# Kernel optimization log

Measured on AMD Instinct MI355X. Metric: run time of the kernel, lower is better.

## Reference

```python
import jax, jax.numpy as jnp
import numpy as np

B, C_IN, C_OUT, K, H, W = 8, 512, 512, 3, 32, 32
EPS = 1e-8


def _fir_filter():
    f1 = jnp.array([1.0, 3.0, 3.0, 1.0], dtype=jnp.float32)
    f = jnp.outer(f1, f1)
    f = f / f.sum()
    return f * 4.0  # gain = 2**2, filter.ndim/2 == 1


def setup_inputs() -> dict:
    key = jax.random.key(0)
    k1, k2, k3 = jax.random.split(key, 3)
    x = jax.random.normal(k1, (B, C_IN, H, W), dtype=jnp.float32)
    styles = jax.random.normal(k2, (B, C_IN), dtype=jnp.float32)
    w = jax.random.normal(k3, (C_OUT, C_IN, K, K), dtype=jnp.float32)  # lr_multiplier=1
    return {"x": x, "styles": styles, "w": w}


def reference(x, styles, w):
    batch = x.shape[0]
    gain = 1.0 / np.sqrt(C_OUT * C_IN * K * K)
    # modulate: [B, O, I, kh, kw]
    wm = (w[None] * gain) * (styles[:, None, :, None, None] + 1.0)
    # demodulate
    dcoefs = jax.lax.rsqrt(jnp.sum(wm * wm, axis=(2, 3, 4)) + EPS)  # [B, O]
    wm = wm * dcoefs[:, :, None, None, None]
    # fused modconv: batch folded into channels/groups
    x1 = x.reshape(1, batch * C_IN, H, W)
    # torch conv_transpose2d(stride=2, padding=0, groups=B) == dilated conv with
    # spatially flipped kernel, lhs_dilation=2, padding=K-1 on each side.
    w_eq = jnp.flip(wm, axis=(-2, -1)).reshape(batch * C_OUT, C_IN, K, K)
    y = jax.lax.conv_general_dilated(
        x1, w_eq,
        window_strides=(1, 1),
        padding=[(K - 1, K - 1), (K - 1, K - 1)],
        lhs_dilation=(2, 2),
        feature_group_count=batch,
        dimension_numbers=("NCHW", "OIHW", "NCHW"),
    )  # [1, B*O, 2H+1, 2W+1]
    # Upfirdn2d: up=1, down=1, pad=[1,1,1,1], depthwise 4x4 FIR (cross-correlation;
    # filter is symmetric so no flip needed)
    C = batch * C_OUT
    f = jnp.broadcast_to(_fir_filter()[None, None], (C, 1, 4, 4))
    y = jax.lax.conv_general_dilated(
        y, f,
        window_strides=(1, 1),
        padding=[(1, 1), (1, 1)],
        feature_group_count=C,
        dimension_numbers=("NCHW", "OIHW", "NCHW"),
    )  # [1, B*O, 2H, 2W]
    return y.reshape(batch, C_OUT, 2 * H, 2 * W)
```

## Files before the change

### kernel.cpp

```cpp
#include <hip/hip_runtime.h>
#include <stdint.h>


#define DI __device__ __forceinline__

typedef __bf16 bf16x8 __attribute__((ext_vector_type(8)));
typedef float f32x4 __attribute__((ext_vector_type(4)));

DI float bf2f(ushort u) { union { uint32_t i; float f; } v; v.i = ((uint32_t)u) << 16; return v.f; }
DI ushort f2bf(float f) {
  union { float f; uint32_t i; } v; v.f = f;
  uint32_t x = v.i;
  return (ushort)((x + 0x7FFFu + ((x >> 16) & 1u)) >> 16);
}

#define GAIN (1.0f / 1536.0f)

__global__ __launch_bounds__(256) void k_wprep(const float* __restrict__ w,
                                               const float* __restrict__ styles,
                                               ushort* __restrict__ Wm) {
  const int o = blockIdx.x;
  const int t = threadIdx.x;
  __shared__ float ss[4096];
  __shared__ float dc[8];
  __shared__ float wred[4][8];
#pragma unroll
  for (int j = 0; j < 4; j++) {
    const int idx = (t + j * 256) * 4;
    *(float4*)&ss[idx] = *(const float4*)&styles[idx];
  }
  float wreg[18];
  const float* wp = w + o * 4608 + t * 18;
#pragma unroll
  for (int k = 0; k < 9; k++) {
    float2 v2 = *(const float2*)(wp + 2 * k);
    wreg[2 * k] = v2.x;
    wreg[2 * k + 1] = v2.y;
  }
  float q0 = 0.f, q1 = 0.f;
#pragma unroll
  for (int k = 0; k < 9; k++) {
    q0 += wreg[k] * wreg[k];
    q1 += wreg[9 + k] * wreg[9 + k];
  }
  __syncthreads();
  float pb[8];
#pragma unroll
  for (int b = 0; b < 8; b++) {
    float s0 = ss[b * 512 + 2 * t] + 1.0f;
    float s1 = ss[b * 512 + 2 * t + 1] + 1.0f;
    pb[b] = s0 * s0 * q0 + s1 * s1 * q1;
  }
#pragma unroll
  for (int b = 0; b < 8; b++)
#pragma unroll
    for (int off = 32; off > 0; off >>= 1) pb[b] += __shfl_down(pb[b], off, 64);
  const int wid = t >> 6, lane = t & 63;
  if (lane == 0) {
#pragma unroll
    for (int b = 0; b < 8; b++) wred[wid][b] = pb[b];
  }
  __syncthreads();
  if (t < 8)
    dc[t] = rsqrtf((wred[0][t] + wred[1][t] + wred[2][t] + wred[3][t]) * (GAIN * GAIN) + 1e-8f);
  __syncthreads();
#pragma unroll
  for (int b = 0; b < 8; b++) {
    const float d = dc[b];
    const float s0 = GAIN * (ss[b * 512 + 2 * t] + 1.0f) * d;
    const float s1 = GAIN * (ss[b * 512 + 2 * t + 1] + 1.0f) * d;
    ushort* base = Wm + ((size_t)(b * 9) * 512 + o) * 512 + 2 * t;
#pragma unroll
    for (int tap = 0; tap < 9; tap++) {
      ushort2 val = make_ushort2(f2bf(wreg[tap] * s0), f2bf(wreg[9 + tap] * s1));
      *(ushort2*)(base + (size_t)tap * 262144) = val;
    }
  }
}

__global__ __launch_bounds__(256) void k_xt(const float* __restrict__ x,
                                            ushort* __restrict__ xt) {
  __shared__ float tl[32][257];
  const int b = blockIdx.z, i0 = blockIdx.y * 32, hw0 = blockIdx.x * 256;
  const int t = threadIdx.x;
  const float* xb = x + b * (512 * 1024);
#pragma unroll
  for (int p = 0; p < 8; p++) {
    const int r = p * 4 + (t >> 6);
    const int c4 = (t & 63) * 4;
    float4 v = *(const float4*)&xb[(i0 + r) * 1024 + hw0 + c4];
    tl[r][c4] = v.x; tl[r][c4 + 1] = v.y; tl[r][c4 + 2] = v.z; tl[r][c4 + 3] = v.w;
  }
  __syncthreads();
  ushort* xtb = xt + b * (1024 * 512);
#pragma unroll
  for (int p = 0; p < 8; p++) {
    const int hw = p * 32 + (t >> 3);
    const int i4 = (t & 7) * 4;
    ushort4 v = make_ushort4(f2bf(tl[i4][hw]), f2bf(tl[i4 + 1][hw]),
                             f2bf(tl[i4 + 2][hw]), f2bf(tl[i4 + 3][hw]));
    *(ushort4*)&xtb[(hw0 + hw) * 512 + i0 + i4] = v;
  }
}

__global__ __launch_bounds__(256) void k_gemm(const ushort* __restrict__ A,
                                              const ushort* __restrict__ Bt,
                                              ushort* __restrict__ C) {
  __shared__ __attribute__((aligned(16))) char smem[32768];
  const int id = blockIdx.x;
  const int batch = id & 7;
  const int rem = id >> 3;
  const int tap = rem >> 5;
  const int t = rem & 31;
  const int mt = t >> 3, nt = t & 7;
  const int g = batch * 9 + tap;
  const ushort* Ag = A + g * (512 * 512);
  const ushort* Bg = Bt + batch * (1024 * 512);
  ushort* Cg = C + g * (512 * 1024);
  const int tid = threadIdx.x;
  const int lane = tid & 63, wv = tid >> 6;
  const int m0 = mt * 128, n0 = nt * 128;
  const int wm2 = wv >> 1, wn2 = wv & 1;
  const int lq = lane >> 4, l15 = lane & 15;
  const int l4 = lane & 3, ld4 = lane >> 2;
  const int r0 = (0 * 4 + wv) * 16 + ld4;
  const int r1 = (1 * 4 + wv) * 16 + ld4;

  const ushort* pA0 = Ag + (m0 + r0) * 512 + l4 * 8;
  const ushort* pA1 = Ag + (m0 + r1) * 512 + l4 * 8;
  const ushort* pB0 = Bg + (n0 + r0) * 512 + l4 * 8;
  const ushort* pB1 = Bg + (n0 + r1) * 512 + l4 * 8;
  char* dA0 = smem + (0 * 4 + wv) * 1024;
  char* dA1 = smem + (1 * 4 + wv) * 1024;
  char* dB0 = smem + 8192 + (0 * 4 + wv) * 1024;
  char* dB1 = smem + 8192 + (1 * 4 + wv) * 1024;

#define ISSUE(buf, kc)                                                                        \
  do {                                                                                        \
    __builtin_amdgcn_global_load_lds((const __attribute__((address_space(1))) void*)(pA0 + (kc)), \
                                     (__attribute__((address_space(3))) void*)(dA0 + (buf)*16384), 16, 0, 0); \
    __builtin_amdgcn_global_load_lds((const __attribute__((address_space(1))) void*)(pA1 + (kc)), \
                                     (__attribute__((address_space(3))) void*)(dA1 + (buf)*16384), 16, 0, 0); \
    __builtin_amdgcn_global_load_lds((const __attribute__((address_space(1))) void*)(pB0 + (kc)), \
                                     (__attribute__((address_space(3))) void*)(dB0 + (buf)*16384), 16, 0, 0); \
    __builtin_amdgcn_global_load_lds((const __attribute__((address_space(1))) void*)(pB1 + (kc)), \
                                     (__attribute__((address_space(3))) void*)(dB1 + (buf)*16384), 16, 0, 0); \
  } while (0)

  const char* abase = smem + (wm2 * 64 + l15) * 64 + lq * 16;
  const char* bbase = smem + 8192 + (wn2 * 64 + l15) * 64 + lq * 16;

  f32x4 zero = {0.f, 0.f, 0.f, 0.f};
  f32x4 acc[4][4];
#pragma unroll
  for (int mi = 0; mi < 4; mi++)
#pragma unroll
    for (int ni = 0; ni < 4; ni++) acc[mi][ni] = zero;

  ISSUE(0, 0);
  for (int it = 0; it < 16; ++it) {
    __syncthreads();
    const int cur = it & 1;
    if (it < 15) ISSUE(cur ^ 1, (it + 1) * 32);
    const int bo = cur * 16384;
    bf16x8 af[4], bfr[4];
#pragma unroll
    for (int mi = 0; mi < 4; mi++) af[mi] = *(const bf16x8*)(abase + bo + mi * 1024);
#pragma unroll
    for (int ni = 0; ni < 4; ni++) bfr[ni] = *(const bf16x8*)(bbase + bo + ni * 1024);
#pragma unroll
    for (int mi = 0; mi < 4; mi++)
#pragma unroll
      for (int ni = 0; ni < 4; ni++)
        acc[mi][ni] = __builtin_amdgcn_mfma_f32_16x16x32_bf16(af[mi], bfr[ni], acc[mi][ni], 0, 0, 0);
  }
#undef ISSUE
  __syncthreads();
  ushort* cs = (ushort*)smem;
#pragma unroll
  for (int mi = 0; mi < 4; mi++) {
#pragma unroll
    for (int ni = 0; ni < 4; ni++) {
      const int row = wm2 * 64 + mi * 16 + lq * 4;
      const int col = wn2 * 64 + ni * 16 + l15;
      f32x4 v = acc[mi][ni];
#pragma unroll
      for (int r = 0; r < 4; r++) cs[(row + r) * 128 + col] = f2bf(v[r]);
    }
  }
  __syncthreads();
#pragma unroll
  for (int p = 0; p < 8; p++) {
    const int r2 = p * 16 + (tid >> 4);
    const int c8 = (tid & 15) * 8;
    *(uint4*)(Cg + (m0 + r2) * 1024 + n0 + c8) = *(const uint4*)(cs + r2 * 128 + c8);
  }
}

__global__ __launch_bounds__(256) void k_fir(const ushort* __restrict__ C,
                                             float* __restrict__ out) {
  const int bo = blockIdx.x;
  const int b = bo >> 9, o = bo & 511;
  __shared__ __attribute__((aligned(16))) ushort Ct[9 * 1024];
  __shared__ float V[3 * 64 * 32];
  const ushort* Cb = C + ((size_t)(b * 9) * 512 + o) * 1024;
  for (int c = threadIdx.x; c < 1152; c += 256) {
    const int tap = c >> 7, off = (c & 127) * 8;
    *(uint4*)&Ct[tap * 1024 + off] = *(const uint4*)&Cb[(size_t)tap * 524288 + off];
  }
  __syncthreads();
#pragma unroll
  for (int j = 0; j < 6; j++) {
    const int gidx = threadIdx.x + j * 256;
    const int kw = gidx >> 9;
    const int rem = gidx & 511;
    const int u = rem >> 3;
    const int w0 = (rem & 7) * 4;
    float a0 = 0.f, a1 = 0.f, a2 = 0.f, a3 = 0.f;
#pragma unroll
    for (int kh = 0; kh < 3; kh++) {
      const int s0 = (kh + 1 + u) & 1;
#pragma unroll
      for (int d = 0; d < 2; d++) {
        const int h = (u + s0 + 2 * d - 1 - kh) >> 1;
        const bool ok = (h >= 0) & (h < 32);
        const float cf = ok ? ((s0 == d) ? 1.f : 3.f) : 0.f;
        const int hh = ok ? h : 0;
        const uint2 cv = *(const uint2*)&Ct[kh * 3072 + kw * 1024 + hh * 32 + w0];
        a0 += cf * bf2f((ushort)(cv.x & 0xffff));
        a1 += cf * bf2f((ushort)(cv.x >> 16));
        a2 += cf * bf2f((ushort)(cv.y & 0xffff));
        a3 += cf * bf2f((ushort)(cv.y >> 16));
      }
    }
    *(float4*)&V[kw * 2048 + u * 32 + w0] = make_float4(a0, a1, a2, a3);
  }
  __syncthreads();
  const size_t ob = (size_t)bo * 4096;
#pragma unroll
  for (int p = 0; p < 4; p++) {
    const int u = p * 16 + (threadIdx.x >> 4);
    const int v0 = (threadIdx.x & 15) * 4;
    float r[4] = {0.f, 0.f, 0.f, 0.f};
#pragma unroll
    for (int q = 0; q < 4; q++) {
      const int v = v0 + q;
#pragma unroll
      for (int kw = 0; kw < 3; kw++) {
        const int t0 = (kw + 1 + v) & 1;
#pragma unroll
        for (int d = 0; d < 2; d++) {
          const int w = (v + t0 + 2 * d - 1 - kw) >> 1;
          const bool ok = (w >= 0) & (w < 32);
          const float cf = ok ? ((t0 == d) ? 1.f : 3.f) : 0.f;
          const int ww = ok ? w : 0;
          r[q] += cf * V[kw * 2048 + u * 32 + ww];
        }
      }
      r[q] *= 0.0625f;
    }
    *(float4*)&out[ob + u * 64 + v0] = make_float4(r[0], r[1], r[2], r[3]);
  }
}

extern "C" void kernel_launch(void* const* d_in, const int* in_sizes, int n_in,
                              void* d_out, int out_size, void* d_ws, size_t ws_size,
                              hipStream_t stream) {
  (void)in_sizes; (void)n_in; (void)out_size; (void)ws_size;
  const float* x = (const float*)d_in[0];
  const float* styles = (const float*)d_in[1];
  const float* w = (const float*)d_in[2];
  float* out = (float*)d_out;
  char* ws = (char*)d_ws;
  ushort* Wm = (ushort*)ws;
  ushort* XT = (ushort*)(ws + 37748736);
  ushort* C = (ushort*)(ws + 37748736 + 8388608);

  k_wprep<<<512, 256, 0, stream>>>(w, styles, Wm);
  k_xt<<<dim3(4, 16, 8), 256, 0, stream>>>(x, XT);
  k_gemm<<<2304, 256, 0, stream>>>(Wm, XT, C);
  k_fir<<<4096, 256, 0, stream>>>(C, out);
}
```

Baseline: 167.0 us.

## Merge prep kernels, pad LDS strides, and widen FIR blocks to 512 threads

Combines the weight-modulation and input-transpose kernels into one launch, using a shared-memory union and splitting work by block index, so one kernel launch and its tail go away. The GEMM epilogue staging buffer gets a padded row stride (136) to cut LDS bank conflicts. The FIR kernel's intermediate buffer is padded (stride 36) and the block grows to 512 threads, halving per-thread loop iterations. The larger FIR blocks and extra LDS may lower occupancy.

```diff
diff --git a/kernel.cpp b/kernel.cpp
--- a/kernel.cpp
+++ b/kernel.cpp
@@ -16,97 +16,99 @@
 
 #define GAIN (1.0f / 1536.0f)
 
-__global__ __launch_bounds__(256) void k_wprep(const float* __restrict__ w,
-                                               const float* __restrict__ styles,
-                                               ushort* __restrict__ Wm) {
-  const int o = blockIdx.x;
+__global__ __launch_bounds__(256) void k_prep(const float* __restrict__ w,
+                                              const float* __restrict__ styles,
+                                              const float* __restrict__ x,
+                                              ushort* __restrict__ Wm,
+                                              ushort* __restrict__ xt) {
+  __shared__ union {
+    struct { float ss[4096]; float dc[8]; float wred[4][8]; } wp;
+    float tl[32][257];
+  } sm;
   const int t = threadIdx.x;
-  __shared__ float ss[4096];
-  __shared__ float dc[8];
-  __shared__ float wred[4][8];
-#pragma unroll
-  for (int j = 0; j < 4; j++) {
-    const int idx = (t + j * 256) * 4;
-    *(float4*)&ss[idx] = *(const float4*)&styles[idx];
-  }
-  float wreg[18];
-  const float* wp = w + o * 4608 + t * 18;
-#pragma unroll
-  for (int k = 0; k < 9; k++) {
-    float2 v2 = *(const float2*)(wp + 2 * k);
-    wreg[2 * k] = v2.x;
-    wreg[2 * k + 1] = v2.y;
-  }
-  float q0 = 0.f, q1 = 0.f;
-#pragma unroll
-  for (int k = 0; k < 9; k++) {
-    q0 += wreg[k] * wreg[k];
-    q1 += wreg[9 + k] * wreg[9 + k];
-  }
-  __syncthreads();
-  float pb[8];
-#pragma unroll
-  for (int b = 0; b < 8; b++) {
-    float s0 = ss[b * 512 + 2 * t] + 1.0f;
-    float s1 = ss[b * 512 + 2 * t + 1] + 1.0f;
-    pb[b] = s0 * s0 * q0 + s1 * s1 * q1;
-  }
-#pragma unroll
-  for (int b = 0; b < 8; b++)
-#pragma unroll
-    for (int off = 32; off > 0; off >>= 1) pb[b] += __shfl_down(pb[b], off, 64);
-  const int wid = t >> 6, lane = t & 63;
-  if (lane == 0) {
-#pragma unroll
-    for (int b = 0; b < 8; b++) wred[wid][b] = pb[b];
-  }
-  __syncthreads();
-  if (t < 8)
-    dc[t] = rsqrtf((wred[0][t] + wred[1][t] + wred[2][t] + wred[3][t]) * (GAIN * GAIN) + 1e-8f);
-  __syncthreads();
-#pragma unroll
-  for (int b = 0; b < 8; b++) {
-    const float d = dc[b];
-    const float s0 = GAIN * (ss[b * 512 + 2 * t] + 1.0f) * d;
-    const float s1 = GAIN * (ss[b * 512 + 2 * t + 1] + 1.0f) * d;
-    ushort* base = Wm + ((size_t)(b * 9) * 512 + o) * 512 + 2 * t;
-#pragma unroll
-    for (int tap = 0; tap < 9; tap++) {
-      ushort2 val = make_ushort2(f2bf(wreg[tap] * s0), f2bf(wreg[9 + tap] * s1));
-      *(ushort2*)(base + (size_t)tap * 262144) = val;
-    }
-  }
-}
-
-__global__ __launch_bounds__(256) void k_xt(const float* __restrict__ x,
-                                            ushort* __restrict__ xt) {
-  __shared__ float tl[32][257];
-  const int b = blockIdx.z, i0 = blockIdx.y * 32, hw0 = blockIdx.x * 256;
-  const int t = threadIdx.x;
-  const float* xb = x + b * (512 * 1024);
-#pragma unroll
-  for (int p = 0; p < 8; p++) {
-    const int r = p * 4 + (t >> 6);
-    const int c4 = (t & 63) * 4;
-    float4 v = *(const float4*)&xb[(i0 + r) * 1024 + hw0 + c4];
-    tl[r][c4] = v.x; tl[r][c4 + 1] = v.y; tl[r][c4 + 2] = v.z; tl[r][c4 + 3] = v.w;
-  }
-  __syncthreads();
-  ushort* xtb = xt + b * (1024 * 512);
-#pragma unroll
-  for (int p = 0; p < 8; p++) {
-    const int hw = p * 32 + (t >> 3);
-    const int i4 = (t & 7) * 4;
-    ushort4 v = make_ushort4(f2bf(tl[i4][hw]), f2bf(tl[i4 + 1][hw]),
-                             f2bf(tl[i4 + 2][hw]), f2bf(tl[i4 + 3][hw]));
-    *(ushort4*)&xtb[(hw0 + hw) * 512 + i0 + i4] = v;
+  if (blockIdx.x < 512) {
+    const int o = blockIdx.x;
+#pragma unroll
+    for (int j = 0; j < 4; j++) {
+      const int idx = (t + j * 256) * 4;
+      *(float4*)&sm.wp.ss[idx] = *(const float4*)&styles[idx];
+    }
+    float wreg[18];
+    const float* wp_ = w + o * 4608 + t * 18;
+#pragma unroll
+    for (int k = 0; k < 9; k++) {
+      float2 v2 = *(const float2*)(wp_ + 2 * k);
+      wreg[2 * k] = v2.x;
+      wreg[2 * k + 1] = v2.y;
+    }
+    float q0 = 0.f, q1 = 0.f;
+#pragma unroll
+    for (int k = 0; k < 9; k++) {
+      q0 += wreg[k] * wreg[k];
+      q1 += wreg[9 + k] * wreg[9 + k];
+    }
+    __syncthreads();
+    float pb[8];
+#pragma unroll
+    for (int b = 0; b < 8; b++) {
+      float s0 = sm.wp.ss[b * 512 + 2 * t] + 1.0f;
+      float s1 = sm.wp.ss[b * 512 + 2 * t + 1] + 1.0f;
+      pb[b] = s0 * s0 * q0 + s1 * s1 * q1;
+    }
+#pragma unroll
+    for (int b = 0; b < 8; b++)
+#pragma unroll
+      for (int off = 32; off > 0; off >>= 1) pb[b] += __shfl_down(pb[b], off, 64);
+    const int wid = t >> 6, lane = t & 63;
+    if (lane == 0) {
+#pragma unroll
+      for (int b = 0; b < 8; b++) sm.wp.wred[wid][b] = pb[b];
+    }
+    __syncthreads();
+    if (t < 8)
+      sm.wp.dc[t] = rsqrtf((sm.wp.wred[0][t] + sm.wp.wred[1][t] + sm.wp.wred[2][t] + sm.wp.wred[3][t]) *
+                               (GAIN * GAIN) + 1e-8f);
+    __syncthreads();
+#pragma unroll
+    for (int b = 0; b < 8; b++) {
+      const float d = sm.wp.dc[b];
+      const float s0 = GAIN * (sm.wp.ss[b * 512 + 2 * t] + 1.0f) * d;
+      const float s1 = GAIN * (sm.wp.ss[b * 512 + 2 * t + 1] + 1.0f) * d;
+      ushort* base = Wm + ((size_t)(b * 9) * 512 + o) * 512 + 2 * t;
+#pragma unroll
+      for (int tap = 0; tap < 9; tap++) {
+        ushort2 val = make_ushort2(f2bf(wreg[tap] * s0), f2bf(wreg[9 + tap] * s1));
+        *(ushort2*)(base + (size_t)tap * 262144) = val;
+      }
+    }
+  } else {
+    const int idx = blockIdx.x - 512;
+    const int hw0 = (idx & 3) * 256, i0 = ((idx >> 2) & 15) * 32, b = idx >> 6;
+    const float* xb = x + b * (512 * 1024);
+#pragma unroll
+    for (int p = 0; p < 8; p++) {
+      const int r = p * 4 + (t >> 6);
+      const int c4 = (t & 63) * 4;
+      float4 v = *(const float4*)&xb[(i0 + r) * 1024 + hw0 + c4];
+      sm.tl[r][c4] = v.x; sm.tl[r][c4 + 1] = v.y; sm.tl[r][c4 + 2] = v.z; sm.tl[r][c4 + 3] = v.w;
+    }
+    __syncthreads();
+    ushort* xtb = xt + b * (1024 * 512);
+#pragma unroll
+    for (int p = 0; p < 8; p++) {
+      const int hw = p * 32 + (t >> 3);
+      const int i4 = (t & 7) * 4;
+      ushort4 v = make_ushort4(f2bf(sm.tl[i4][hw]), f2bf(sm.tl[i4 + 1][hw]),
+                               f2bf(sm.tl[i4 + 2][hw]), f2bf(sm.tl[i4 + 3][hw]));
+      *(ushort4*)&xtb[(hw0 + hw) * 512 + i0 + i4] = v;
+    }
   }
 }
 
 __global__ __launch_bounds__(256) void k_gemm(const ushort* __restrict__ A,
                                               const ushort* __restrict__ Bt,
                                               ushort* __restrict__ C) {
-  __shared__ __attribute__((aligned(16))) char smem[32768];
+  __shared__ __attribute__((aligned(16))) char smem[34816];
   const int id = blockIdx.x;
   const int batch = id & 7;
   const int rem = id >> 3;
@@ -185,7 +187,7 @@
       const int col = wn2 * 64 + ni * 16 + l15;
       f32x4 v = acc[mi][ni];
 #pragma unroll
-      for (int r = 0; r < 4; r++) cs[(row + r) * 128 + col] = f2bf(v[r]);
+      for (int r = 0; r < 4; r++) cs[(row + r) * 136 + col] = f2bf(v[r]);
     }
   }
   __syncthreads();
@@ -193,25 +195,25 @@
   for (int p = 0; p < 8; p++) {
     const int r2 = p * 16 + (tid >> 4);
     const int c8 = (tid & 15) * 8;
-    *(uint4*)(Cg + (m0 + r2) * 1024 + n0 + c8) = *(const uint4*)(cs + r2 * 128 + c8);
-  }
-}
-
-__global__ __launch_bounds__(256) void k_fir(const ushort* __restrict__ C,
+    *(uint4*)(Cg + (m0 + r2) * 1024 + n0 + c8) = *(const uint4*)(cs + r2 * 136 + c8);
+  }
+}
+
+__global__ __launch_bounds__(512) void k_fir(const ushort* __restrict__ C,
                                              float* __restrict__ out) {
   const int bo = blockIdx.x;
   const int b = bo >> 9, o = bo & 511;
   __shared__ __attribute__((aligned(16))) ushort Ct[9 * 1024];
-  __shared__ float V[3 * 64 * 32];
+  __shared__ float V[3 * 64 * 36];
   const ushort* Cb = C + ((size_t)(b * 9) * 512 + o) * 1024;
-  for (int c = threadIdx.x; c < 1152; c += 256) {
+  for (int c = threadIdx.x; c < 1152; c += 512) {
     const int tap = c >> 7, off = (c & 127) * 8;
     *(uint4*)&Ct[tap * 1024 + off] = *(const uint4*)&Cb[(size_t)tap * 524288 + off];
   }
   __syncthreads();
 #pragma unroll
-  for (int j = 0; j < 6; j++) {
-    const int gidx = threadIdx.x + j * 256;
+  for (int j = 0; j < 3; j++) {
+    const int gidx = threadIdx.x + j * 512;
     const int kw = gidx >> 9;
     const int rem = gidx & 511;
     const int u = rem >> 3;
@@ -233,14 +235,15 @@
         a3 += cf * bf2f((ushort)(cv.y >> 16));
       }
     }
-    *(float4*)&V[kw * 2048 + u * 32 + w0] = make_float4(a0, a1, a2, a3);
+    *(float4*)&V[kw * 2304 + u * 36 + w0] = make_float4(a0, a1, a2, a3);
   }
   __syncthreads();
   const size_t ob = (size_t)bo * 4096;
 #pragma unroll
-  for (int p = 0; p < 4; p++) {
-    const int u = p * 16 + (threadIdx.x >> 4);
-    const int v0 = (threadIdx.x & 15) * 4;
+  for (int j = 0; j < 2; j++) {
+    const int px4 = threadIdx.x + j * 512;
+    const int u = px4 >> 4;
+    const int v0 = (px4 & 15) * 4;
     float r[4] = {0.f, 0.f, 0.f, 0.f};
 #pragma unroll
     for (int q = 0; q < 4; q++) {
@@ -250,11 +253,11 @@
         const int t0 = (kw + 1 + v) & 1;
 #pragma unroll
         for (int d = 0; d < 2; d++) {
-          const int w = (v + t0 + 2 * d - 1 - kw) >> 1;
-          const bool ok = (w >= 0) & (w < 32);
+          const int wx = (v + t0 + 2 * d - 1 - kw) >> 1;
+          const bool ok = (wx >= 0) & (wx < 32);
           const float cf = ok ? ((t0 == d) ? 1.f : 3.f) : 0.f;
-          const int ww = ok ? w : 0;
-          r[q] += cf * V[kw * 2048 + u * 32 + ww];
+          const int ww = ok ? wx : 0;
+          r[q] += cf * V[kw * 2304 + u * 36 + ww];
         }
       }
       r[q] *= 0.0625f;
@@ -276,8 +279,7 @@
   ushort* XT = (ushort*)(ws + 37748736);
   ushort* C = (ushort*)(ws + 37748736 + 8388608);
 
-  k_wprep<<<512, 256, 0, stream>>>(w, styles, Wm);
-  k_xt<<<dim3(4, 16, 8), 256, 0, stream>>>(x, XT);
+  k_prep<<<1024, 256, 0, stream>>>(w, styles, x, Wm, XT);
   k_gemm<<<2304, 256, 0, stream>>>(Wm, XT, C);
-  k_fir<<<4096, 256, 0, stream>>>(C, out);
-}
+  k_fir<<<4096, 512, 0, stream>>>(C, out);
+}
```

Measured after the change: 158.2 us. 5.3% less time.
